# Optimization experiments

Hardware: AMD Instinct MI355X
Metric: run time of the kernel (lower is better)

## Reference

```python
import jax, jax.numpy as jnp
import numpy as np

START_DISP, END_DISP = 0, 192
STEP = 3
D0 = np.arange(START_DISP // 4, END_DISP // 4, STEP)  # [16] coarse disparities (1/4 res)
D1 = np.arange(-STEP + 1, STEP)                        # [5] refinement offsets


def _build_volume(feat_l, feat_r, disps):
    # Vectorized equivalent of AnyNet._build_volume_2d: for each disparity d,
    # left features at cols [0,W), right features shifted to cols [d, W+d).
    B, C, H, W = feat_l.shape
    md = int(disps.max())
    Wc = W + md
    D = len(disps)
    left = jnp.pad(feat_l, ((0, 0), (0, 0), (0, 0), (0, md)))          # [B,C,H,Wc]
    left = jnp.broadcast_to(left[:, None], (B, D, C, H, Wc))           # [B,D,C,H,Wc]
    idx = np.arange(Wc)[None, :] - disps[:, None]                      # [D,Wc] source col
    valid = jnp.asarray((idx >= 0) & (idx < W), feat_l.dtype)          # [D,Wc]
    right = feat_r[:, :, :, np.clip(idx, 0, W - 1)]                    # [B,C,H,D,Wc]
    right = jnp.transpose(right, (0, 3, 1, 2, 4)) * valid[None, :, None, None, :]
    return jnp.concatenate([left, right], axis=2)                      # [B,D,2C,H,Wc]


def _disparity_regression(x, disps):
    # disparity values, sum over channel axis (dim=2, keepdim).
    w = jax.nn.softmax(x, axis=1)
    d = jnp.asarray(disps, x.dtype).reshape(1, -1, 1, 1, 1)
    return jnp.sum(w * d, axis=2, keepdims=True)                       # [B,D,1,H,Wc]


def setup_inputs() -> dict:
    key = jax.random.key(0)
    k1, k2 = jax.random.split(key)
    B, C, H, W = 2, 64, 128, 240
    return {
        "feats_l": jax.random.normal(k1, (B, C, H, W), jnp.float32),
        "feats_r": jax.random.normal(k2, (B, C, H, W), jnp.float32),
    }


def reference(feats_l, feats_r):
    cost0 = _build_volume(feats_l, feats_r, D0)        # [2,16,128,128,285]
    disp_re_1 = _disparity_regression(cost0, D0)       # [2,16,1,128,285]
    cost1 = _build_volume(feats_l, feats_r, D1)        # [2,5,128,128,242]
    disp_re_2 = _disparity_regression(cost1, D1)       # [2,5,1,128,242]
    return disp_re_1, disp_re_2
```

## Files before the change

### kernel.cpp

```cpp
#include <hip/hip_runtime.h>

namespace {
constexpr int kB   = 2;
constexpr int kC   = 64;
constexpr int kH   = 128;
constexpr int kW   = 240;
constexpr int kD0  = 16;
constexpr int kD1  = 5;
constexpr int kWc1 = 285;
constexpr int kWc2 = 242;
constexpr int kPad = 48;
constexpr int kRow = 336;
constexpr int kCP  = 32;
constexpr int kGroups   = 3;
constexpr int kGThreads = 320;
constexpr int kThreads  = kGroups * kGThreads;
constexpr int kAcc  = kD0 + kD1;
constexpr int kRStr = kWc1 * kAcc;
constexpr int kOut1 = kB * kD0 * kH * kWc1;
constexpr int kN1   = kD0 * kWc1;
constexpr int kN2   = kD1 * kWc2;
typedef unsigned int v2u __attribute__((ext_vector_type(2)));
typedef float v2f __attribute__((ext_vector_type(2)));

__device__ __forceinline__ v2f UP(unsigned int x) {
  v2f f;
  f.x = __uint_as_float(x << 16);
  f.y = __uint_as_float(x & 0xffff0000u);
  return f;
}
__device__ __forceinline__ unsigned int pk2(float lo, float hi) {
  unsigned int r;
  asm("v_cvt_pk_bf16_f32 %0, %1, %2" : "=v"(r) : "v"(lo), "v"(hi));
  return r;
}
__device__ __forceinline__ v2f pfma(v2f a, v2f b, v2f c) {
  return __builtin_elementwise_fma(a, b, c);
}
}

__global__ __launch_bounds__(kThreads)
void anynet_disp_kernel(const float* __restrict__ fr, float* __restrict__ out) {
  __shared__ unsigned int E[kCP * kRow];
  __shared__ float P[kGroups * kRStr];
  const int bh  = blockIdx.x;
  const int b   = bh >> 7;
  const int h   = bh & 127;
  const int tid = threadIdx.x;

  const float* fr_b = fr + (size_t)b * kC * kH * kW + (size_t)h * kW;
  const int i0 = tid, i1 = tid + kThreads;
  const int cp0 = i0 / 60, xq0 = i0 % 60;
  const int cp1 = i1 / 60, xq1 = i1 % 60;
  const float4 a0 = *reinterpret_cast<const float4*>(
      fr_b + (size_t)(2 * cp0) * (kH * kW) + 4 * xq0);
  const float4 b0 = *reinterpret_cast<const float4*>(
      fr_b + (size_t)(2 * cp0 + 1) * (kH * kW) + 4 * xq0);
  const float4 a1 = *reinterpret_cast<const float4*>(
      fr_b + (size_t)(2 * cp1) * (kH * kW) + 4 * xq1);
  const float4 b1 = *reinterpret_cast<const float4*>(
      fr_b + (size_t)(2 * cp1 + 1) * (kH * kW) + 4 * xq1);
  if (tid < kCP * 24) {
    const int cp = tid / 24, q = tid % 24;
    const int j4 = (q < 12) ? q : q + 60;
    const uint4 ones = {0x3F803F80u, 0x3F803F80u, 0x3F803F80u, 0x3F803F80u};
    *reinterpret_cast<uint4*>(&E[cp * kRow + 4 * j4]) = ones;
  }
  {
    uint4 w0;
    w0.x = pk2(__expf(a0.x), __expf(b0.x));
    w0.y = pk2(__expf(a0.y), __expf(b0.y));
    w0.z = pk2(__expf(a0.z), __expf(b0.z));
    w0.w = pk2(__expf(a0.w), __expf(b0.w));
    *reinterpret_cast<uint4*>(&E[cp0 * kRow + kPad + 4 * xq0]) = w0;
    uint4 w1;
    w1.x = pk2(__expf(a1.x), __expf(b1.x));
    w1.y = pk2(__expf(a1.y), __expf(b1.y));
    w1.z = pk2(__expf(a1.z), __expf(b1.z));
    w1.w = pk2(__expf(a1.w), __expf(b1.w));
    *reinterpret_cast<uint4*>(&E[cp1 * kRow + kPad + 4 * xq1]) = w1;
  }
  __syncthreads();

  const int g = tid / kGThreads;
  const int t = tid % kGThreads;
  v2f acc1[kD0] = {};
  v2f acc2[kD1] = {};
  if (t < kWc1) {
    const int cbeg = (g == 0) ? 0 : (g == 1 ? 11 : 22);
    const int clen = (g < 2) ? 11 : 10;
    unsigned int addr = (unsigned int)(uintptr_t)(const void*)&E[cbeg * kRow + t + 3];
    for (int cc = 0; cc < clen; ++cc) {
      v2u p0, p1, p2, p3, p4, p5, p6, p7, q0, q1;
      asm volatile(
          "ds_read2_b32 %0, %10 offset0:45 offset1:42\n\t"
          "ds_read2_b32 %1, %10 offset0:39 offset1:36\n\t"
          "ds_read2_b32 %2, %10 offset0:33 offset1:30\n\t"
          "ds_read2_b32 %3, %10 offset0:27 offset1:24\n\t"
          "ds_read2_b32 %4, %10 offset0:21 offset1:18\n\t"
          "ds_read2_b32 %5, %10 offset0:15 offset1:12\n\t"
          "ds_read2_b32 %6, %10 offset0:9 offset1:6\n\t"
          "ds_read2_b32 %7, %10 offset0:3 offset1:0\n\t"
          "ds_read2_b32 %8, %10 offset0:43 offset1:44\n\t"
          "ds_read2_b32 %9, %10 offset0:46 offset1:47\n\t"
          "s_waitcnt lgkmcnt(0)"
          : "=&v"(p0), "=&v"(p1), "=&v"(p2), "=&v"(p3), "=&v"(p4),
            "=&v"(p5), "=&v"(p6), "=&v"(p7), "=&v"(q0), "=&v"(q1)
          : "v"(addr));
      const v2f f0  = UP(p0.x), f1  = UP(p0.y), f2  = UP(p1.x), f3  = UP(p1.y);
      const v2f f4  = UP(p2.x), f5  = UP(p2.y), f6  = UP(p3.x), f7  = UP(p3.y);
      const v2f f8  = UP(p4.x), f9  = UP(p4.y), f10 = UP(p5.x), f11 = UP(p5.y);
      const v2f f12 = UP(p6.x), f13 = UP(p6.y), f14 = UP(p7.x), f15 = UP(p7.y);
      const v2f e0 = UP(q0.x), e1 = UP(q0.y);
      const v2f e2 = UP(q1.x), e3 = UP(q1.y);
      const v2f s = (((f0 + f1) + (f2 + f3)) + ((f4 + f5) + (f6 + f7))) +
                    (((f8 + f9) + (f10 + f11)) + ((f12 + f13) + (f14 + f15)));
      v2f r;
      r.x = __builtin_amdgcn_rcpf(s.x);
      r.y = __builtin_amdgcn_rcpf(s.y);
      acc1[0]  = pfma(f0,  r, acc1[0]);   acc1[1]  = pfma(f1,  r, acc1[1]);
      acc1[2]  = pfma(f2,  r, acc1[2]);   acc1[3]  = pfma(f3,  r, acc1[3]);
      acc1[4]  = pfma(f4,  r, acc1[4]);   acc1[5]  = pfma(f5,  r, acc1[5]);
      acc1[6]  = pfma(f6,  r, acc1[6]);   acc1[7]  = pfma(f7,  r, acc1[7]);
      acc1[8]  = pfma(f8,  r, acc1[8]);   acc1[9]  = pfma(f9,  r, acc1[9]);
      acc1[10] = pfma(f10, r, acc1[10]);  acc1[11] = pfma(f11, r, acc1[11]);
      acc1[12] = pfma(f12, r, acc1[12]);  acc1[13] = pfma(f13, r, acc1[13]);
      acc1[14] = pfma(f14, r, acc1[14]);  acc1[15] = pfma(f15, r, acc1[15]);
      const v2f s2 = ((e0 + e1) + (e2 + e3)) + f0;
      v2f r2;
      r2.x = __builtin_amdgcn_rcpf(s2.x);
      r2.y = __builtin_amdgcn_rcpf(s2.y);
      acc2[0] = pfma(e3, r2, acc2[0]);
      acc2[1] = pfma(e2, r2, acc2[1]);
      acc2[2] = pfma(f0, r2, acc2[2]);
      acc2[3] = pfma(e1, r2, acc2[3]);
      acc2[4] = pfma(e0, r2, acc2[4]);
      addr += kRow * 4;
    }
  }
  __syncthreads();

  if (t < kWc1) {
    float* __restrict__ R = &P[g * kRStr + t * kAcc];
    #pragma unroll
    for (int k = 0; k < kD0; ++k) R[k] = acc1[k].x + acc1[k].y;
    #pragma unroll
    for (int j = 0; j < kD1; ++j) R[kD0 + j] = acc2[j].x + acc2[j].y;
  }
  __syncthreads();

  for (int i = tid; i < kN1 + kN2; i += kThreads) {
    if (i < kN1) {
      const int d   = i / kWc1;
      const int col = i % kWc1;
      const int o   = col * kAcc + d;
      const float v = P[o] + P[kRStr + o] + P[2 * kRStr + o];
      out[((b * kD0 + d) * kH + h) * kWc1 + col] =
          (3.0f * (float)d) * (4.0f + v);
    } else {
      const int i2  = i - kN1;
      const int j   = i2 / kWc2;
      const int col = i2 % kWc2;
      const int o   = col * kAcc + kD0 + j;
      const float v = P[o] + P[kRStr + o] + P[2 * kRStr + o];
      out[kOut1 + ((b * kD1 + j) * kH + h) * kWc2 + col] =
          (float)(j - 2) * (64.0f / 5.0f + v);
    }
  }
}

extern "C" void kernel_launch(void* const* d_in, const int* in_sizes, int n_in,
                              void* d_out, int out_size, void* d_ws, size_t ws_size,
                              hipStream_t stream) {
  const float* feat_r = (const float*)d_in[1];
  float* out = (float*)d_out;
  anynet_disp_kernel<<<dim3(kB * kH), dim3(kThreads), 0, stream>>>(feat_r, out);
}
```

Baseline: 17.26 us.

## Split each image row into two column halves per block to double grid size

Each block now handles one (batch, row) pair and only half of the output columns, with a halo of right-feature columns loaded into a smaller LDS tile. Out-of-range columns are filled with exp(0)=1 padding, and the launch becomes 512 blocks of 512 threads with a minimum of 4 blocks per SM/CU requested in launch bounds. The aim is better CU occupancy and load balance than one large block per row. The cost is redundant halo loads and exps, 32 idle threads per block, and extra bounds checks on the output writes.

```diff
diff --git a/kernel.cpp b/kernel.cpp
--- a/kernel.cpp
+++ b/kernel.cpp
@@ -10,16 +10,18 @@
 constexpr int kWc1 = 285;
 constexpr int kWc2 = 242;
 constexpr int kPad = 48;
-constexpr int kRow = 336;
+constexpr int kCols = 144;
+constexpr int kRowL = 196;
+constexpr int kF4   = kRowL / 4;
 constexpr int kCP  = 32;
 constexpr int kGroups   = 3;
-constexpr int kGThreads = 320;
-constexpr int kThreads  = kGroups * kGThreads;
+constexpr int kGThreads = 160;
+constexpr int kThreads  = 512;
 constexpr int kAcc  = kD0 + kD1;
-constexpr int kRStr = kWc1 * kAcc;
+constexpr int kSlot = kCols * kAcc;
 constexpr int kOut1 = kB * kD0 * kH * kWc1;
-constexpr int kN1   = kD0 * kWc1;
-constexpr int kN2   = kD1 * kWc2;
+constexpr int kN1   = kD0 * kCols;
+constexpr int kN2   = kD1 * kCols;
 typedef unsigned int v2u __attribute__((ext_vector_type(2)));
 typedef float v2f __attribute__((ext_vector_type(2)));
 
@@ -39,46 +41,51 @@
 }
 }
 
-__global__ __launch_bounds__(kThreads)
+__global__ __launch_bounds__(kThreads, 4)
 void anynet_disp_kernel(const float* __restrict__ fr, float* __restrict__ out) {
-  __shared__ unsigned int E[kCP * kRow];
-  __shared__ float P[kGroups * kRStr];
-  const int bh  = blockIdx.x;
-  const int b   = bh >> 7;
-  const int h   = bh & 127;
-  const int tid = threadIdx.x;
+  __shared__ unsigned int E[kCP * kRowL];
+  __shared__ float P[kGroups * kSlot];
+  const int blk  = blockIdx.x;
+  const int half = blk & 1;
+  const int bh   = blk >> 1;
+  const int b    = bh >> 7;
+  const int h    = bh & 127;
+  const int colbeg = half * kCols;
+  const int tid  = threadIdx.x;
 
   const float* fr_b = fr + (size_t)b * kC * kH * kW + (size_t)h * kW;
-  const int i0 = tid, i1 = tid + kThreads;
-  const int cp0 = i0 / 60, xq0 = i0 % 60;
-  const int cp1 = i1 / 60, xq1 = i1 % 60;
-  const float4 a0 = *reinterpret_cast<const float4*>(
-      fr_b + (size_t)(2 * cp0) * (kH * kW) + 4 * xq0);
-  const float4 b0 = *reinterpret_cast<const float4*>(
-      fr_b + (size_t)(2 * cp0 + 1) * (kH * kW) + 4 * xq0);
-  const float4 a1 = *reinterpret_cast<const float4*>(
-      fr_b + (size_t)(2 * cp1) * (kH * kW) + 4 * xq1);
-  const float4 b1 = *reinterpret_cast<const float4*>(
-      fr_b + (size_t)(2 * cp1 + 1) * (kH * kW) + 4 * xq1);
-  if (tid < kCP * 24) {
-    const int cp = tid / 24, q = tid % 24;
-    const int j4 = (q < 12) ? q : q + 60;
-    const uint4 ones = {0x3F803F80u, 0x3F803F80u, 0x3F803F80u, 0x3F803F80u};
-    *reinterpret_cast<uint4*>(&E[cp * kRow + 4 * j4]) = ones;
-  }
   {
-    uint4 w0;
-    w0.x = pk2(__expf(a0.x), __expf(b0.x));
-    w0.y = pk2(__expf(a0.y), __expf(b0.y));
-    w0.z = pk2(__expf(a0.z), __expf(b0.z));
-    w0.w = pk2(__expf(a0.w), __expf(b0.w));
-    *reinterpret_cast<uint4*>(&E[cp0 * kRow + kPad + 4 * xq0]) = w0;
-    uint4 w1;
-    w1.x = pk2(__expf(a1.x), __expf(b1.x));
-    w1.y = pk2(__expf(a1.y), __expf(b1.y));
-    w1.z = pk2(__expf(a1.z), __expf(b1.z));
-    w1.w = pk2(__expf(a1.w), __expf(b1.w));
-    *reinterpret_cast<uint4*>(&E[cp1 * kRow + kPad + 4 * xq1]) = w1;
+    float4 la[4], lb[4];
+    int item[4];
+    #pragma unroll
+    for (int u = 0; u < 4; ++u) {
+      const int i = tid + u * kThreads;
+      item[u] = i;
+      const int cp = i / kF4, lq = i % kF4;
+      const int x0 = colbeg - kPad + 4 * lq;
+      const int xc = (x0 < 0) ? 0 : (x0 > kW - 4 ? kW - 4 : x0);
+      const size_t base = (size_t)(2 * (cp & 31)) * (kH * kW) + xc;
+      la[u] = *reinterpret_cast<const float4*>(fr_b + base);
+      lb[u] = *reinterpret_cast<const float4*>(fr_b + base + (kH * kW));
+    }
+    #pragma unroll
+    for (int u = 0; u < 4; ++u) {
+      const int i = item[u];
+      if (i < kCP * kF4) {
+        const int cp = i / kF4, lq = i % kF4;
+        const int x0 = colbeg - kPad + 4 * lq;
+        uint4 w;
+        if (x0 >= 0 && x0 + 3 < kW) {
+          w.x = pk2(__expf(la[u].x), __expf(lb[u].x));
+          w.y = pk2(__expf(la[u].y), __expf(lb[u].y));
+          w.z = pk2(__expf(la[u].z), __expf(lb[u].z));
+          w.w = pk2(__expf(la[u].w), __expf(lb[u].w));
+        } else {
+          w = uint4{0x3F803F80u, 0x3F803F80u, 0x3F803F80u, 0x3F803F80u};
+        }
+        *reinterpret_cast<uint4*>(&E[cp * kRowL + 4 * lq]) = w;
+      }
+    }
   }
   __syncthreads();
 
@@ -86,10 +93,10 @@
   const int t = tid % kGThreads;
   v2f acc1[kD0] = {};
   v2f acc2[kD1] = {};
-  if (t < kWc1) {
+  if (g < kGroups && t < kCols) {
     const int cbeg = (g == 0) ? 0 : (g == 1 ? 11 : 22);
     const int clen = (g < 2) ? 11 : 10;
-    unsigned int addr = (unsigned int)(uintptr_t)(const void*)&E[cbeg * kRow + t + 3];
+    unsigned int addr = (unsigned int)(uintptr_t)(const void*)&E[cbeg * kRowL + t + 3];
     for (int cc = 0; cc < clen; ++cc) {
       v2u p0, p1, p2, p3, p4, p5, p6, p7, q0, q1;
       asm volatile(
@@ -135,13 +142,13 @@
       acc2[2] = pfma(f0, r2, acc2[2]);
       acc2[3] = pfma(e1, r2, acc2[3]);
       acc2[4] = pfma(e0, r2, acc2[4]);
-      addr += kRow * 4;
+      addr += kRowL * 4;
     }
   }
   __syncthreads();
 
-  if (t < kWc1) {
-    float* __restrict__ R = &P[g * kRStr + t * kAcc];
+  if (g < kGroups && t < kCols) {
+    float* __restrict__ R = &P[g * kSlot + t * kAcc];
     #pragma unroll
     for (int k = 0; k < kD0; ++k) R[k] = acc1[k].x + acc1[k].y;
     #pragma unroll
@@ -151,20 +158,26 @@
 
   for (int i = tid; i < kN1 + kN2; i += kThreads) {
     if (i < kN1) {
-      const int d   = i / kWc1;
-      const int col = i % kWc1;
-      const int o   = col * kAcc + d;
-      const float v = P[o] + P[kRStr + o] + P[2 * kRStr + o];
-      out[((b * kD0 + d) * kH + h) * kWc1 + col] =
-          (3.0f * (float)d) * (4.0f + v);
+      const int d  = i / kCols;
+      const int t2 = i % kCols;
+      const int col = colbeg + t2;
+      if (col < kWc1) {
+        const int o = t2 * kAcc + d;
+        const float v = P[o] + P[kSlot + o] + P[2 * kSlot + o];
+        out[((b * kD0 + d) * kH + h) * kWc1 + col] =
+            (3.0f * (float)d) * (4.0f + v);
+      }
     } else {
-      const int i2  = i - kN1;
-      const int j   = i2 / kWc2;
-      const int col = i2 % kWc2;
-      const int o   = col * kAcc + kD0 + j;
-      const float v = P[o] + P[kRStr + o] + P[2 * kRStr + o];
-      out[kOut1 + ((b * kD1 + j) * kH + h) * kWc2 + col] =
-          (float)(j - 2) * (64.0f / 5.0f + v);
+      const int i2 = i - kN1;
+      const int j  = i2 / kCols;
+      const int t2 = i2 % kCols;
+      const int col = colbeg + t2;
+      if (col < kWc2) {
+        const int o = t2 * kAcc + kD0 + j;
+        const float v = P[o] + P[kSlot + o] + P[2 * kSlot + o];
+        out[kOut1 + ((b * kD1 + j) * kH + h) * kWc2 + col] =
+            (float)(j - 2) * (64.0f / 5.0f + v);
+      }
     }
   }
 }
@@ -174,5 +187,5 @@
                               hipStream_t stream) {
   const float* feat_r = (const float*)d_in[1];
   float* out = (float*)d_out;
-  anynet_disp_kernel<<<dim3(kB * kH), dim3(kThreads), 0, stream>>>(feat_r, out);
+  anynet_disp_kernel<<<dim3(kB * kH * 2), dim3(kThreads), 0, stream>>>(feat_r, out);
 }
```

Result: slower. 18.50 us (+7.1%).
